# Optimization experiments

Measured on AMD Instinct MI355X. Metric: run time of the kernel, lower is better.

Reference implementation:

```python
import jax, jax.numpy as jnp
import numpy as np

B, D, F, M = 4096, 768, 16384, 256

def setup_inputs() -> dict:
    key = jax.random.key(0)
    ks = jax.random.split(key, 5)
    return {
        "x": jax.random.normal(ks[0], (B, D), dtype=jnp.float32),
        "memory_bank": jax.random.normal(ks[1], (F, D), dtype=jnp.float32),
        "W_q": jax.random.normal(ks[2], (M, D), dtype=jnp.float32) / np.sqrt(D),
        "b_q": jnp.zeros((M,), dtype=jnp.float32),
        "W_k": jax.random.normal(ks[3], (M, D), dtype=jnp.float32) / np.sqrt(D),
        "b_k": jnp.zeros((M,), dtype=jnp.float32),
        "W_v": jax.random.normal(ks[4], (D, D), dtype=jnp.float32) / np.sqrt(D),
        "b_v": jnp.zeros((D,), dtype=jnp.float32),
        "temperature": jnp.full((1,), np.sqrt(M / 4.0), dtype=jnp.float32),
    }

def reference(x, memory_bank, W_q, b_q, W_k, b_k, W_v, b_v, temperature):
    # Q from x, K/V from fixed memory bank (torch Linear: y = x @ W.T + b)
    Q = x @ W_q.T + b_q                     # [B, M]
    K = memory_bank @ W_k.T + b_k           # [F, M]
    V = memory_bank @ W_v.T + b_v           # [F, D]
    scores = (Q @ K.T) / temperature        # [B, F]
    f = jax.nn.softmax(scores, axis=1)      # max-subtraction folded into stable softmax
    x_hat = f @ V                           # [B, D]
    return (x, x_hat, f, V)
```

## Files before the change

### kernel.cpp

```cpp
#include <hip/hip_runtime.h>
#include <stdint.h>

#define B_ 4096
#define D_ 768
#define F_ 16384
#define M_ 256

typedef short bf16x8 __attribute__((ext_vector_type(8)));
typedef float f32x4 __attribute__((ext_vector_type(4)));
typedef unsigned short ushort8 __attribute__((ext_vector_type(8)));

__device__ __forceinline__ unsigned short f2bf(float f) {
  union { float f; uint32_t u; } c; c.f = f;
  uint32_t u = c.u;
  uint32_t r = (u + 0x7FFFu + ((u >> 16) & 1u)) >> 16;
  return (unsigned short)r;
}

__device__ __forceinline__ float bf2f(unsigned short s) {
  union { uint32_t u; float f; } c; c.u = ((uint32_t)s) << 16;
  return c.f;
}

__device__ __forceinline__ void gl_lds16(const void* g, void* l) {
  __builtin_amdgcn_global_load_lds(
      (const __attribute__((address_space(1))) unsigned int*)g,
      (__attribute__((address_space(3))) unsigned int*)l, 16, 0, 0);
}

__global__ void cast_kernel(const float* __restrict__ in, unsigned short* __restrict__ out,
                            float* __restrict__ cpy, int n4) {
  int i = blockIdx.x * blockDim.x + threadIdx.x;
  if (i >= n4) return;
  float4 v = reinterpret_cast<const float4*>(in)[i];
  ushort4 u;
  u.x = f2bf(v.x); u.y = f2bf(v.y); u.z = f2bf(v.z); u.w = f2bf(v.w);
  reinterpret_cast<ushort4*>(out)[i] = u;
  if (cpy) reinterpret_cast<float4*>(cpy)[i] = v;
}

template <int EPI>
__global__ __launch_bounds__(256, 2) void gemm_bt(
    const unsigned short* __restrict__ A, const unsigned short* __restrict__ Bm,
    const float* __restrict__ bias, float* __restrict__ Cf,
    unsigned short* __restrict__ Cb, int M, int N, int K,
    float* __restrict__ rowsum, const float* __restrict__ tptr) {
  __shared__ unsigned short As[128 * 32];
  __shared__ unsigned short Bs[128 * 32];
  const int tid = threadIdx.x, lane = tid & 63, wave = tid >> 6;
  const int m0 = blockIdx.y * 128, n0 = blockIdx.x * 128;
  const int wr = wave >> 1, wc = wave & 1;
  const int q = lane >> 4;
  f32x4 acc[4][4] = {};

  for (int k0 = 0; k0 < K; k0 += 32) {
#pragma unroll
    for (int i = 0; i < 2; ++i) {
      int cb = (i * 4 + wave) * 64;
      int ch = cb + lane;
      int row = ch >> 2, ko = (ch & 3) * 8;
      gl_lds16(A + (size_t)(m0 + row) * K + k0 + ko, (char*)As + (size_t)cb * 16);
      gl_lds16(Bm + (size_t)(n0 + row) * K + k0 + ko, (char*)Bs + (size_t)cb * 16);
    }
    __syncthreads();
    bf16x8 a[4];
#pragma unroll
    for (int m = 0; m < 4; ++m)
      a[m] = *reinterpret_cast<const bf16x8*>(
          &As[(wr * 64 + m * 16 + (lane & 15)) * 32 + q * 8]);
#pragma unroll
    for (int n = 0; n < 4; ++n) {
      bf16x8 b = *reinterpret_cast<const bf16x8*>(
          &Bs[(wc * 64 + n * 16 + (lane & 15)) * 32 + q * 8]);
#pragma unroll
      for (int m = 0; m < 4; ++m)
        acc[m][n] = __builtin_amdgcn_mfma_f32_16x16x32_bf16(a[m], b, acc[m][n], 0, 0, 0);
    }
    __syncthreads();
  }

  const int rbase = m0 + wr * 64 + q * 4;
  const int cbase = n0 + wc * 64 + (lane & 15);
  if (EPI == 2 || EPI == 3) {
    const float invt = 1.0f / tptr[0];
    const int mb = m0 >> 7, t0 = n0 >> 5;
#pragma unroll
    for (int m = 0; m < 4; ++m) {
      float rs[4] = {0.f, 0.f, 0.f, 0.f};
#pragma unroll
      for (int n = 0; n < 4; ++n) {
        int col = cbase + n * 16;
        int tl = wc * 2 + (n >> 1);
        int slot = ((lane & 15) >> 3) + (n & 1) * 2;
        int off = lane & 7;
#pragma unroll
        for (int r = 0; r < 4; ++r) {
          float e = __expf(acc[m][n][r] * invt);
          rs[r] += e;
          if (EPI == 2) {
            Cf[(size_t)(rbase + m * 16 + r) * N + col] = e;
          } else {
            int rl = (rbase - m0) + m * 16 + r;
            int p = slot ^ ((rl >> 1) & 3);
            Cb[((size_t)(mb * 512 + t0 + tl)) * 4096 + rl * 32 + p * 8 + off] = f2bf(e);
          }
        }
      }
#pragma unroll
      for (int r = 0; r < 4; ++r) {
        float s = rs[r];
        s += __shfl_xor(s, 1);
        s += __shfl_xor(s, 2);
        s += __shfl_xor(s, 4);
        s += __shfl_xor(s, 8);
        if ((lane & 15) == 0) atomicAdd(&rowsum[rbase + m * 16 + r], s);
      }
    }
  } else {
#pragma unroll
    for (int m = 0; m < 4; ++m) {
#pragma unroll
      for (int n = 0; n < 4; ++n) {
        int col = cbase + n * 16;
        float bv = bias[col];
#pragma unroll
        for (int r = 0; r < 4; ++r) {
          float v = acc[m][n][r] + bv;
          size_t idx = (size_t)(rbase + m * 16 + r) * N + col;
          if (EPI == 0) Cb[idx] = f2bf(v);
          else Cf[idx] = v;
        }
      }
    }
  }
}

__global__ __launch_bounds__(256) void vt_tiler(const float* __restrict__ V,
                                                unsigned short* __restrict__ Vt_tiled) {
  __shared__ unsigned short T[768][36];
  const int t = blockIdx.x, k0 = t * 32, tid = threadIdx.x;
  const int kl = tid >> 3, c0 = (tid & 7) * 4;
  for (int cb = 0; cb < 768; cb += 32) {
    float4 v = *reinterpret_cast<const float4*>(&V[(size_t)(k0 + kl) * D_ + cb + c0]);
    T[cb + c0 + 0][kl] = f2bf(v.x);
    T[cb + c0 + 1][kl] = f2bf(v.y);
    T[cb + c0 + 2][kl] = f2bf(v.z);
    T[cb + c0 + 3][kl] = f2bf(v.w);
  }
  __syncthreads();
  for (int d = tid; d < 768; d += 256) {
    const int x = (d >> 1) & 3;
    unsigned short* o = Vt_tiled + (size_t)t * 24576 + d * 32;
#pragma unroll
    for (int s = 0; s < 4; ++s) {
      ushort4 lo = *reinterpret_cast<const ushort4*>(&T[d][(s ^ x) * 8]);
      ushort4 hi = *reinterpret_cast<const ushort4*>(&T[d][(s ^ x) * 8 + 4]);
      *reinterpret_cast<ushort4*>(o + s * 8) = lo;
      *reinterpret_cast<ushort4*>(o + s * 8 + 4) = hi;
    }
  }
}

__global__ __launch_bounds__(256, 2) void xhat_clean(
    const unsigned short* __restrict__ Et, const unsigned short* __restrict__ Vtt,
    const float* __restrict__ rowsum, unsigned short* __restrict__ partial) {
  __shared__ unsigned short As[128 * 32];
  __shared__ unsigned short Bs[192 * 32];
  const int tid = threadIdx.x, lane = tid & 63, wave = tid >> 6;
  const int combo = blockIdx.x & 15, mb = blockIdx.x >> 4;
  const int ks = combo >> 2, nb = combo & 3;
  const int q = lane >> 4;
  const int wr = wave >> 1, wc = wave & 1;
  const int t0 = ks * 128;
  f32x4 acc[4][6] = {};

  const unsigned short* asrc =
      Et + ((size_t)mb * 512 + t0) * 4096 + (wave * 2) * 512 + lane * 8;
  const unsigned short* bsrc =
      Vtt + (size_t)t0 * 24576 + nb * 192 * 32 + (wave * 3) * 512 + lane * 8;

  for (int si = 0; si < 128; ++si) {
#pragma unroll
    for (int j = 0; j < 2; ++j)
      gl_lds16(asrc + (size_t)si * 4096 + j * 512,
               (char*)As + (size_t)(wave * 2 + j) * 1024);
#pragma unroll
    for (int j = 0; j < 3; ++j)
      gl_lds16(bsrc + (size_t)si * 24576 + j * 512,
               (char*)Bs + (size_t)(wave * 3 + j) * 1024);
    __syncthreads();
    bf16x8 a[4], b[6];
#pragma unroll
    for (int m = 0; m < 4; ++m) {
      int R = wr * 64 + m * 16 + (lane & 15);
      a[m] = *reinterpret_cast<const bf16x8*>(&As[R * 32 + ((q ^ ((R >> 1) & 3)) * 8)]);
    }
#pragma unroll
    for (int n = 0; n < 6; ++n) {
      int C = wc * 96 + n * 16 + (lane & 15);
      b[n] = *reinterpret_cast<const bf16x8*>(&Bs[C * 32 + ((q ^ ((C >> 1) & 3)) * 8)]);
    }
#pragma unroll
    for (int n = 0; n < 6; ++n)
#pragma unroll
      for (int m = 0; m < 4; ++m)
        acc[m][n] = __builtin_amdgcn_mfma_f32_16x16x32_bf16(a[m], b[n], acc[m][n], 0, 0, 0);
    __syncthreads();
  }

  unsigned short* P = partial + (size_t)ks * B_ * D_;
#pragma unroll
  for (int m = 0; m < 4; ++m) {
    int rowb = mb * 128 + wr * 64 + m * 16 + q * 4;
#pragma unroll
    for (int r = 0; r < 4; ++r) {
      float inv = 1.0f / rowsum[rowb + r];
      size_t ro = (size_t)(rowb + r) * D_;
#pragma unroll
      for (int n = 0; n < 6; ++n) {
        int col = nb * 192 + wc * 96 + n * 16 + (lane & 15);
        P[ro + col] = f2bf(acc[m][n][r] * inv);
      }
    }
  }
}

__global__ __launch_bounds__(256) void normalize_f(
    const unsigned short* __restrict__ Et, const float* __restrict__ rowsum,
    float* __restrict__ f) {
  int u = blockIdx.x * blockDim.x + threadIdx.x;
  int g = u >> 9, w = u & 511;
  int r = w >> 2, p = w & 3;
  int rb = g >> 9, t = g & 511;
  int row = rb * 128 + r;
  int col = t * 32 + (p ^ ((r >> 1) & 3)) * 8;
  float inv = 1.0f / rowsum[row];
  ushort8 e = *reinterpret_cast<const ushort8*>(&Et[(size_t)g * 4096 + w * 8]);
  float4 o0, o1;
  o0.x = bf2f(e[0]) * inv; o0.y = bf2f(e[1]) * inv;
  o0.z = bf2f(e[2]) * inv; o0.w = bf2f(e[3]) * inv;
  o1.x = bf2f(e[4]) * inv; o1.y = bf2f(e[5]) * inv;
  o1.z = bf2f(e[6]) * inv; o1.w = bf2f(e[7]) * inv;
  float* fp = &f[(size_t)row * F_ + col];
  *reinterpret_cast<float4*>(fp) = o0;
  *reinterpret_cast<float4*>(fp + 4) = o1;
}

__global__ __launch_bounds__(512, 4) void xhat_v4(
    float* __restrict__ Ef, const unsigned short* __restrict__ Vt_tiled,
    const float* __restrict__ rowsum, unsigned short* __restrict__ partial) {
  __shared__ unsigned short As2[64 * 32];
  __shared__ unsigned short Vs[768 * 32];
  const int tid = threadIdx.x, lane = tid & 63, wave = tid >> 6;
  const int ks = blockIdx.x & 7, rb = blockIdx.x >> 3;
  const int r0 = rb * 64;
  const int kbeg = ks * (F_ / 8);
  const int wr = wave >> 2, wc = wave & 3;
  const int erow = tid >> 3, ec = (tid & 7) * 4;
  const float inv_f = 1.0f / rowsum[r0 + erow];
  const int q = lane >> 4;
  f32x4 acc[2][12] = {};

  float* ep = Ef + (size_t)(r0 + erow) * F_ + kbeg + ec;
  float4 e = *reinterpret_cast<const float4*>(ep);
  const int NSTEP = (F_ / 8) / 32;
  const unsigned short* vt_base =
      Vt_tiled + (size_t)(kbeg >> 5) * 24576 + wave * 512 + lane * 8;

  for (int si = 0; si < NSTEP; ++si) {
    float4 f4 = make_float4(e.x * inv_f, e.y * inv_f, e.z * inv_f, e.w * inv_f);
    *reinterpret_cast<float4*>(ep) = f4;
    ushort4 u;
    u.x = f2bf(e.x); u.y = f2bf(e.y); u.z = f2bf(e.z); u.w = f2bf(e.w);
    {
      int slot = ec >> 3, off = ec & 7;
      *reinterpret_cast<ushort4*>(
          &As2[erow * 32 + ((slot ^ ((erow >> 1) & 3)) * 8) + off]) = u;
    }
    const unsigned short* vs_src = vt_base + (size_t)si * 24576;
#pragma unroll
    for (int j = 0; j < 6; ++j)
      gl_lds16(vs_src + j * 4096, (char*)Vs + (size_t)(j * 512 + wave * 64) * 16);
    __syncthreads();
    if (si + 1 < NSTEP) e = *reinterpret_cast<const float4*>(ep + 32);
    ep += 32;
    bf16x8 a[2];
#pragma unroll
    for (int m = 0; m < 2; ++m) {
      int R = wr * 32 + m * 16 + (lane & 15);
      a[m] = *reinterpret_cast<const bf16x8*>(&As2[R * 32 + ((q ^ ((R >> 1) & 3)) * 8)]);
    }
#pragma unroll
    for (int n = 0; n < 12; ++n) {
      int C = wc * 192 + n * 16 + (lane & 15);
      bf16x8 b = *reinterpret_cast<const bf16x8*>(&Vs[C * 32 + ((q ^ ((C >> 1) & 3)) * 8)]);
      acc[0][n] = __builtin_amdgcn_mfma_f32_16x16x32_bf16(a[0], b, acc[0][n], 0, 0, 0);
      acc[1][n] = __builtin_amdgcn_mfma_f32_16x16x32_bf16(a[1], b, acc[1][n], 0, 0, 0);
    }
    __syncthreads();
  }

  unsigned short* P = partial + (size_t)ks * B_ * D_;
#pragma unroll
  for (int m = 0; m < 2; ++m) {
    int rowb = r0 + wr * 32 + m * 16 + q * 4;
#pragma unroll
    for (int r = 0; r < 4; ++r) {
      float inv = 1.0f / rowsum[rowb + r];
      size_t row_off = (size_t)(rowb + r) * D_;
#pragma unroll
      for (int n = 0; n < 12; ++n) {
        int col = wc * 192 + n * 16 + (lane & 15);
        P[row_off + col] = f2bf(acc[m][n][r] * inv);
      }
    }
  }
}

__global__ void reduce_kernel(const unsigned short* __restrict__ partial,
                              float* __restrict__ out, int n8, int nks) {
  int i = blockIdx.x * blockDim.x + threadIdx.x;
  if (i >= n8) return;
  size_t base = (size_t)i * 8;
  float s[8] = {0.f, 0.f, 0.f, 0.f, 0.f, 0.f, 0.f, 0.f};
  for (int ks = 0; ks < nks; ++ks) {
    ushort8 v = *reinterpret_cast<const ushort8*>(&partial[(size_t)ks * B_ * D_ + base]);
#pragma unroll
    for (int j = 0; j < 8; ++j) s[j] += bf2f(v[j]);
  }
  float4 o0 = make_float4(s[0], s[1], s[2], s[3]);
  float4 o1 = make_float4(s[4], s[5], s[6], s[7]);
  *reinterpret_cast<float4*>(&out[base]) = o0;
  *reinterpret_cast<float4*>(&out[base + 4]) = o1;
}

extern "C" void kernel_launch(void* const* d_in, const int* in_sizes, int n_in,
                              void* d_out, int out_size, void* d_ws, size_t ws_size,
                              hipStream_t stream) {
  const float* x = (const float*)d_in[0];
  const float* mb = (const float*)d_in[1];
  const float* Wq = (const float*)d_in[2];
  const float* bq = (const float*)d_in[3];
  const float* Wk = (const float*)d_in[4];
  const float* bk = (const float*)d_in[5];
  const float* Wv = (const float*)d_in[6];
  const float* bv = (const float*)d_in[7];
  const float* temp = (const float*)d_in[8];

  float* out_x = (float*)d_out;
  float* out_xhat = out_x + (size_t)B_ * D_;
  float* out_f = out_xhat + (size_t)B_ * D_;
  float* out_V = out_f + (size_t)B_ * F_;

  char* ws = (char*)d_ws;
  const size_t WS_NEED_NEW = 195051520;

  if (ws_size >= WS_NEED_NEW) {
    unsigned short* Qb  = (unsigned short*)(ws + 0);
    unsigned short* Kb  = (unsigned short*)(ws + 2097152);
    unsigned short* Vtt = (unsigned short*)(ws + 10485760);
    float* rowsum       = (float*)(ws + 35651584);
    char* A0 = ws + 35667968;
    unsigned short* xb  = (unsigned short*)(A0 + 0);
    unsigned short* mbb = (unsigned short*)(A0 + 6291456);
    unsigned short* Wqb = (unsigned short*)(A0 + 31457280);
    unsigned short* Wkb = (unsigned short*)(A0 + 31850496);
    unsigned short* Wvb = (unsigned short*)(A0 + 32243712);
    unsigned short* Et  = (unsigned short*)A0;
    unsigned short* partial = (unsigned short*)(ws + 169885696);

    hipMemsetAsync(rowsum, 0, B_ * sizeof(float), stream);

    cast_kernel<<<(B_ * D_ / 4 + 255) / 256, 256, 0, stream>>>(x, xb, out_x, B_ * D_ / 4);
    cast_kernel<<<(F_ * D_ / 4 + 255) / 256, 256, 0, stream>>>(mb, mbb, nullptr, F_ * D_ / 4);
    cast_kernel<<<(M_ * D_ / 4 + 255) / 256, 256, 0, stream>>>(Wq, Wqb, nullptr, M_ * D_ / 4);
    cast_kernel<<<(M_ * D_ / 4 + 255) / 256, 256, 0, stream>>>(Wk, Wkb, nullptr, M_ * D_ / 4);
    cast_kernel<<<(D_ * D_ / 4 + 255) / 256, 256, 0, stream>>>(Wv, Wvb, nullptr, D_ * D_ / 4);

    dim3 blk(256);
    gemm_bt<0><<<dim3(M_ / 128, B_ / 128), blk, 0, stream>>>(xb, Wqb, bq, nullptr, Qb,
                                                             B_, M_, D_, nullptr, nullptr);
    gemm_bt<0><<<dim3(M_ / 128, F_ / 128), blk, 0, stream>>>(mbb, Wkb, bk, nullptr, Kb,
                                                             F_, M_, D_, nullptr, nullptr);
    gemm_bt<1><<<dim3(D_ / 128, F_ / 128), blk, 0, stream>>>(mbb, Wvb, bv, out_V, nullptr,
                                                             F_, D_, D_, nullptr, nullptr);
    vt_tiler<<<dim3(F_ / 32), 256, 0, stream>>>(out_V, Vtt);
    gemm_bt<3><<<dim3(F_ / 128, B_ / 128), blk, 0, stream>>>(Qb, Kb, nullptr, nullptr, Et,
                                                             B_, F_, M_, rowsum, temp);
    normalize_f<<<dim3(B_ * F_ / 8 / 256), 256, 0, stream>>>(Et, rowsum, out_f);
    xhat_clean<<<dim3(512), dim3(256), 0, stream>>>(Et, Vtt, rowsum, partial);
    reduce_kernel<<<(B_ * D_ / 8 + 255) / 256, 256, 0, stream>>>(partial, out_xhat,
                                                                 B_ * D_ / 8, 4);
  } else {
    unsigned short* xb  = (unsigned short*)(ws + 0);
    unsigned short* mbb = (unsigned short*)(ws + 6291456);
    unsigned short* Wqb = (unsigned short*)(ws + 31457280);
    unsigned short* Wkb = (unsigned short*)(ws + 31850496);
    unsigned short* Wvb = (unsigned short*)(ws + 32243712);
    unsigned short* Qb  = (unsigned short*)(ws + 33423360);
    unsigned short* Kb  = (unsigned short*)(ws + 35520512);
    unsigned short* Vtt = (unsigned short*)(ws + 43909120);
    float* rowsum       = (float*)(ws + 69074944);
    unsigned short* partial = (unsigned short*)(ws + 69091328);

    hipMemsetAsync(rowsum, 0, B_ * sizeof(float), stream);

    cast_kernel<<<(B_ * D_ / 4 + 255) / 256, 256, 0, stream>>>(x, xb, out_x, B_ * D_ / 4);
    cast_kernel<<<(F_ * D_ / 4 + 255) / 256, 256, 0, stream>>>(mb, mbb, nullptr, F_ * D_ / 4);
    cast_kernel<<<(M_ * D_ / 4 + 255) / 256, 256, 0, stream>>>(Wq, Wqb, nullptr, M_ * D_ / 4);
    cast_kernel<<<(M_ * D_ / 4 + 255) / 256, 256, 0, stream>>>(Wk, Wkb, nullptr, M_ * D_ / 4);
    cast_kernel<<<(D_ * D_ / 4 + 255) / 256, 256, 0, stream>>>(Wv, Wvb, nullptr, D_ * D_ / 4);

    dim3 blk(256);
    gemm_bt<0><<<dim3(M_ / 128, B_ / 128), blk, 0, stream>>>(xb, Wqb, bq, nullptr, Qb,
                                                             B_, M_, D_, nullptr, nullptr);
    gemm_bt<0><<<dim3(M_ / 128, F_ / 128), blk, 0, stream>>>(mbb, Wkb, bk, nullptr, Kb,
                                                             F_, M_, D_, nullptr, nullptr);
    gemm_bt<1><<<dim3(D_ / 128, F_ / 128), blk, 0, stream>>>(mbb, Wvb, bv, out_V, nullptr,
                                                             F_, D_, D_, nullptr, nullptr);
    vt_tiler<<<dim3(F_ / 32), 256, 0, stream>>>(out_V, Vtt);
    gemm_bt<2><<<dim3(F_ / 128, B_ / 128), blk, 0, stream>>>(Qb, Kb, nullptr, out_f, nullptr,
                                                             B_, F_, M_, rowsum, temp);
    xhat_v4<<<dim3(512), dim3(512), 0, stream>>>(out_f, Vtt, rowsum, partial);
    reduce_kernel<<<(B_ * D_ / 8 + 255) / 256, 256, 0, stream>>>(partial, out_xhat,
                                                                 B_ * D_ / 8, 8);
  }
}
```

Measured before the change: 464.5 us.

## Stage exp tile in LDS for coalesced stores; widen xhat kernel to 512 threads

The EPI==3 epilogue of the scores GEMM now writes bf16 exponentials into a 128x128 LDS tile, then stores them to the swizzled tiled layout with coalesced 16-byte vector writes instead of scattered 2-byte stores. The xhat GEMM doubles its block to 8 waves, splitting the 192-column tile four ways. It loads two K-steps per barrier pair, with separate waves fetching A and B, which halves the loop trip count and the number of syncs. The changes add 32KB of LDS to the scores GEMM and raise register and LDS pressure per block in the xhat kernel, which could reduce occupancy.

```diff
diff --git a/kernel.cpp b/kernel.cpp
--- a/kernel.cpp
+++ b/kernel.cpp
@@ -81,29 +81,55 @@
 
   const int rbase = m0 + wr * 64 + q * 4;
   const int cbase = n0 + wc * 64 + (lane & 15);
-  if (EPI == 2 || EPI == 3) {
+  if constexpr (EPI == 3) {
+    __shared__ unsigned short Cs[128 * 128];
     const float invt = 1.0f / tptr[0];
-    const int mb = m0 >> 7, t0 = n0 >> 5;
+    const int rl0 = wr * 64 + q * 4, cl0 = wc * 64 + (lane & 15);
 #pragma unroll
     for (int m = 0; m < 4; ++m) {
       float rs[4] = {0.f, 0.f, 0.f, 0.f};
 #pragma unroll
       for (int n = 0; n < 4; ++n) {
-        int col = cbase + n * 16;
-        int tl = wc * 2 + (n >> 1);
-        int slot = ((lane & 15) >> 3) + (n & 1) * 2;
-        int off = lane & 7;
 #pragma unroll
         for (int r = 0; r < 4; ++r) {
           float e = __expf(acc[m][n][r] * invt);
           rs[r] += e;
-          if (EPI == 2) {
-            Cf[(size_t)(rbase + m * 16 + r) * N + col] = e;
-          } else {
-            int rl = (rbase - m0) + m * 16 + r;
-            int p = slot ^ ((rl >> 1) & 3);
-            Cb[((size_t)(mb * 512 + t0 + tl)) * 4096 + rl * 32 + p * 8 + off] = f2bf(e);
-          }
+          Cs[(rl0 + m * 16 + r) * 128 + cl0 + n * 16] = f2bf(e);
+        }
+      }
+#pragma unroll
+      for (int r = 0; r < 4; ++r) {
+        float s = rs[r];
+        s += __shfl_xor(s, 1);
+        s += __shfl_xor(s, 2);
+        s += __shfl_xor(s, 4);
+        s += __shfl_xor(s, 8);
+        if ((lane & 15) == 0) atomicAdd(&rowsum[rbase + m * 16 + r], s);
+      }
+    }
+    __syncthreads();
+    const size_t ebase = ((size_t)(m0 >> 7) * 512 + (n0 >> 5)) * 4096;
+#pragma unroll
+    for (int j = 0; j < 8; ++j) {
+      int u = j * 256 + tid;
+      int tl = u >> 9, r = (u >> 2) & 127, p = u & 3;
+      ushort8 v = *reinterpret_cast<const ushort8*>(
+          &Cs[r * 128 + tl * 32 + ((p ^ ((r >> 1) & 3)) * 8)]);
+      *reinterpret_cast<ushort8*>(&Cb[ebase + (size_t)tl * 4096 + r * 32 + p * 8]) = v;
+    }
+  } else if constexpr (EPI == 2) {
+    const float invt = 1.0f / tptr[0];
+#pragma unroll
+    for (int m = 0; m < 4; ++m) {
+      float rs[4] = {0.f, 0.f, 0.f, 0.f};
+#pragma unroll
+      for (int n = 0; n < 4; ++n) {
+        int col = cbase + n * 16;
+#pragma unroll
+        for (int r = 0; r < 4; ++r) {
+          float e = __expf(acc[m][n][r] * invt);
+          Cf[(size_t)(rbase + m * 16 + r) * N + col] = e;
+          rs[r] += e;
         }
       }
 #pragma unroll
@@ -161,50 +187,66 @@
   }
 }
 
-__global__ __launch_bounds__(256, 2) void xhat_clean(
+__global__ __launch_bounds__(512, 4) void xhat_clean(
     const unsigned short* __restrict__ Et, const unsigned short* __restrict__ Vtt,
     const float* __restrict__ rowsum, unsigned short* __restrict__ partial) {
-  __shared__ unsigned short As[128 * 32];
-  __shared__ unsigned short Bs[192 * 32];
+  __shared__ unsigned short As[2][128 * 32];
+  __shared__ unsigned short Bs[2][192 * 32];
   const int tid = threadIdx.x, lane = tid & 63, wave = tid >> 6;
   const int combo = blockIdx.x & 15, mb = blockIdx.x >> 4;
   const int ks = combo >> 2, nb = combo & 3;
   const int q = lane >> 4;
-  const int wr = wave >> 1, wc = wave & 1;
+  const int wr = wave >> 2, wc = wave & 3;
   const int t0 = ks * 128;
-  f32x4 acc[4][6] = {};
-
-  const unsigned short* asrc =
-      Et + ((size_t)mb * 512 + t0) * 4096 + (wave * 2) * 512 + lane * 8;
-  const unsigned short* bsrc =
-      Vtt + (size_t)t0 * 24576 + nb * 192 * 32 + (wave * 3) * 512 + lane * 8;
-
-  for (int si = 0; si < 128; ++si) {
-#pragma unroll
-    for (int j = 0; j < 2; ++j)
-      gl_lds16(asrc + (size_t)si * 4096 + j * 512,
-               (char*)As + (size_t)(wave * 2 + j) * 1024);
-#pragma unroll
-    for (int j = 0; j < 3; ++j)
-      gl_lds16(bsrc + (size_t)si * 24576 + j * 512,
-               (char*)Bs + (size_t)(wave * 3 + j) * 1024);
-    __syncthreads();
-    bf16x8 a[4], b[6];
-#pragma unroll
-    for (int m = 0; m < 4; ++m) {
-      int R = wr * 64 + m * 16 + (lane & 15);
-      a[m] = *reinterpret_cast<const bf16x8*>(&As[R * 32 + ((q ^ ((R >> 1) & 3)) * 8)]);
-    }
-#pragma unroll
-    for (int n = 0; n < 6; ++n) {
-      int C = wc * 96 + n * 16 + (lane & 15);
-      b[n] = *reinterpret_cast<const bf16x8*>(&Bs[C * 32 + ((q ^ ((C >> 1) & 3)) * 8)]);
-    }
-#pragma unroll
-    for (int n = 0; n < 6; ++n)
-#pragma unroll
-      for (int m = 0; m < 4; ++m)
-        acc[m][n] = __builtin_amdgcn_mfma_f32_16x16x32_bf16(a[m], b[n], acc[m][n], 0, 0, 0);
+  f32x4 acc[4][3] = {};
+
+  const unsigned short* abase =
+      Et + ((size_t)mb * 512 + t0) * 4096 + lane * 8;
+  const unsigned short* bbase =
+      Vtt + (size_t)t0 * 24576 + nb * 6144 + lane * 8;
+
+  for (int si = 0; si < 64; ++si) {
+    const size_t tA = (size_t)(2 * si) * 4096;
+    const size_t tB = (size_t)(2 * si) * 24576;
+    if (wave < 4) {
+#pragma unroll
+      for (int j = 0; j < 4; ++j) {
+        int c = wave * 4 + j;
+        int h = c >> 3, cw = c & 7;
+        gl_lds16(abase + tA + (size_t)h * 4096 + cw * 512,
+                 (char*)As + h * 8192 + cw * 1024);
+      }
+    } else {
+#pragma unroll
+      for (int j = 0; j < 6; ++j) {
+        int c = (wave - 4) * 6 + j;
+        int h = c / 12, cc = c % 12;
+        gl_lds16(bbase + tB + (size_t)h * 24576 + cc * 512,
+                 (char*)Bs + h * 12288 + cc * 1024);
+      }
+    }
+    __syncthreads();
+#pragma unroll
+    for (int h = 0; h < 2; ++h) {
+      bf16x8 a[4], b[3];
+#pragma unroll
+      for (int m = 0; m < 4; ++m) {
+        int R = wr * 64 + m * 16 + (lane & 15);
+        a[m] = *reinterpret_cast<const bf16x8*>(
+            &As[h][R * 32 + ((q ^ ((R >> 1) & 3)) * 8)]);
+      }
+#pragma unroll
+      for (int n = 0; n < 3; ++n) {
+        int C = wc * 48 + n * 16 + (lane & 15);
+        b[n] = *reinterpret_cast<const bf16x8*>(
+            &Bs[h][C * 32 + ((q ^ ((C >> 1) & 3)) * 8)]);
+      }
+#pragma unroll
+      for (int n = 0; n < 3; ++n)
+#pragma unroll
+        for (int m = 0; m < 4; ++m)
+          acc[m][n] = __builtin_amdgcn_mfma_f32_16x16x32_bf16(a[m], b[n], acc[m][n], 0, 0, 0);
+    }
     __syncthreads();
   }
 
@@ -217,8 +259,8 @@
       float inv = 1.0f / rowsum[rowb + r];
       size_t ro = (size_t)(rowb + r) * D_;
 #pragma unroll
-      for (int n = 0; n < 6; ++n) {
-        int col = nb * 192 + wc * 96 + n * 16 + (lane & 15);
+      for (int n = 0; n < 3; ++n) {
+        int col = nb * 192 + wc * 48 + n * 16 + (lane & 15);
         P[ro + col] = f2bf(acc[m][n][r] * inv);
       }
     }
@@ -388,7 +430,7 @@
     gemm_bt<3><<<dim3(F_ / 128, B_ / 128), blk, 0, stream>>>(Qb, Kb, nullptr, nullptr, Et,
                                                              B_, F_, M_, rowsum, temp);
     normalize_f<<<dim3(B_ * F_ / 8 / 256), 256, 0, stream>>>(Et, rowsum, out_f);
-    xhat_clean<<<dim3(512), dim3(256), 0, stream>>>(Et, Vtt, rowsum, partial);
+    xhat_clean<<<dim3(512), dim3(512), 0, stream>>>(Et, Vtt, rowsum, partial);
     reduce_kernel<<<(B_ * D_ / 8 + 255) / 256, 256, 0, stream>>>(partial, out_xhat,
                                                                  B_ * D_ / 8, 4);
   } else {
```

Result: no change. 464.0 us (-0.1%).
